# Kernel tuning notes

Hardware: AMD Instinct MI355X
Metric: run time of the kernel (lower is better)

The kernel has to match this reference:

```python
import jax, jax.numpy as jnp
import numpy as np
from jax import lax


def setup_inputs() -> dict:
    key = jax.random.key(0)
    k1, k2 = jax.random.split(key)
    L, B, D = 1024, 16, 1024
    x = jax.random.normal(k1, (L, B, D), dtype=jnp.float32)
    # weight maps n_in -> n_out*k with k=3 (n_in == n_out); small scale for stability
    weight = jax.random.normal(k2, (D, 3 * D), dtype=jnp.float32) * 0.05
    bias = jnp.zeros((2 * D,), dtype=jnp.float32)
    c0 = jnp.zeros((B, D), dtype=jnp.float32)
    return {"x": x, "weight": weight, "bias": bias, "c0": c0}


def reference(x, weight, bias, c0):
    # SRUCell forward, k == 3 (n_in == n_out), unidirectional, tanh activation,
    # no dropout masks (mask_h == NULL -> mask = 1).
    L, B, D = x.shape
    u = (x.reshape(L * B, D) @ weight).reshape(L, B, D, 3)
    b1 = bias[:D]
    b2 = bias[D:]
    u0 = u[..., 0]                                   # [L, B, D]
    g1 = jax.nn.sigmoid(u[..., 1] + b1)              # forget gate
    g2 = jax.nn.sigmoid(u[..., 2] + b2)              # reset/highway gate

    def step(c, inp):
        u0_t, g1_t, g2_t, x_t = inp
        c_new = (c - u0_t) * g1_t + u0_t             # c = c'*g1 + u0*(1-g1)
        h_t = (jnp.tanh(c_new) - x_t) * g2_t + x_t   # h = act(c)*g2 + x*(1-g2)
        return c_new, h_t

    c_last, h = lax.scan(step, c0, (u0, g1, g2, x))
    return h, c_last
```

## Files before the change

### kernel.cpp

```cpp
#include <hip/hip_runtime.h>

#define L_DIM 1024
#define B_DIM 16
#define D_DIM 1024
#define K_DIM 1024
#define N_DIM 3072
#define M_DIM (L_DIM * B_DIM)
#define CHAINS 16384
#define CHUNK 32
#define NCHUNK 32

typedef float f32x4 __attribute__((ext_vector_type(4)));
typedef __bf16 bf16x8 __attribute__((ext_vector_type(8)));
typedef unsigned short u16;
typedef unsigned int u32;

__device__ __forceinline__ u16 f2bf(float f) {
  u32 u = __float_as_uint(f);
  u = u + 0x7FFFu + ((u >> 16) & 1u);
  return (u16)(u >> 16);
}
__device__ __forceinline__ float bf2f(u16 v) {
  return __uint_as_float(((u32)v) << 16);
}
__device__ __forceinline__ float bf2f_lo(u32 v) {
  return __uint_as_float(v << 16);
}
__device__ __forceinline__ float bf2f_hi(u32 v) {
  return __uint_as_float(v & 0xffff0000u);
}
__device__ __forceinline__ float fexp(float v) {
  return __builtin_amdgcn_exp2f(v * 1.4426950408889634f);
}
__device__ __forceinline__ float sigm(float z) {
  return __builtin_amdgcn_rcpf(1.0f + fexp(-z));
}
__device__ __forceinline__ float ftanh(float v) {
  return 1.0f - 2.0f * __builtin_amdgcn_rcpf(1.0f + fexp(2.0f * v));
}

__global__ __launch_bounds__(256) void cvt_x_kernel(const float4* __restrict__ in,
                                                    ushort4* __restrict__ out, int n4) {
  int i = blockIdx.x * 256 + threadIdx.x;
  if (i < n4) {
    float4 v = in[i];
    ushort4 o;
    o.x = f2bf(v.x); o.y = f2bf(v.y); o.z = f2bf(v.z); o.w = f2bf(v.w);
    out[i] = o;
  }
}

__global__ __launch_bounds__(256) void cvt_w_kernel(const float* __restrict__ W,
                                                    u16* __restrict__ Wt) {
  __shared__ float tile[64][65];
  int c0 = blockIdx.x * 64;
  int r0 = blockIdx.y * 64;
  int tx = threadIdx.x & 63;
  int ty = threadIdx.x >> 6;
#pragma unroll
  for (int i = 0; i < 16; ++i) {
    int row = i * 4 + ty;
    tile[row][tx] = W[(size_t)(r0 + row) * N_DIM + c0 + tx];
  }
  __syncthreads();
#pragma unroll
  for (int i = 0; i < 16; ++i) {
    int crow = i * 4 + ty;
    int c = c0 + crow;
    int nprime = (c % 3) * D_DIM + (c / 3);
    Wt[(size_t)nprime * K_DIM + r0 + tx] = f2bf(tile[tx][crow]);
  }
}


#define AS1 __attribute__((address_space(1)))
#define AS3 __attribute__((address_space(3)))
#define STAGE(gp, lp) do { \
  __builtin_amdgcn_global_load_lds((const AS1 void*)(gp), (AS3 void*)(lp), 16, 0, 0); \
  __builtin_amdgcn_global_load_lds((const AS1 void*)((gp) + (size_t)64 * K_DIM), \
                                   (AS3 void*)((lp) + 4096), 16, 0, 0); \
} while (0)

#define QUAD(AI, JB, BF) \
  _Pragma("unroll") \
  for (int i = 0; i < 4; ++i) { \
    _Pragma("unroll") \
    for (int j = 0; j < 2; ++j) { \
      acc[AI + i][JB + j] = __builtin_amdgcn_mfma_f32_16x16x32_bf16(aF[i][0], BF[j][0], acc[AI + i][JB + j], 0, 0, 0); \
      acc[AI + i][JB + j] = __builtin_amdgcn_mfma_f32_16x16x32_bf16(aF[i][1], BF[j][1], acc[AI + i][JB + j], 0, 0, 0); \
    } \
  }

__global__ __launch_bounds__(512, 2) void gemm_kernel(const u16* __restrict__ A,
                                                      const u16* __restrict__ Bt,
                                                      u16* __restrict__ U) {
  __shared__ __align__(16) u16 sm[65536];
  const int tid = threadIdx.x;
  const int wave = tid >> 6;
  const int lane = tid & 63;
  const int wm = wave >> 2;
  const int wn = wave & 3;
  const int quad = lane >> 4;
  const int l16 = lane & 15;

  const int flat = blockIdx.y * 12 + blockIdx.x;
  const int swz = (flat & 7) * 96 + (flat >> 3);
  const int m0 = (swz / 12) * 256;
  const int n0 = (swz % 12) * 256;

  const int rr = tid >> 3;
  const int slot = (tid & 7) ^ (rr & 7);
  const u16* gA = A + (size_t)(m0 + rr) * K_DIM + slot * 8;
  const u16* gB = Bt + (size_t)(n0 + rr) * K_DIM + slot * 8;

  u16* ldsA = sm + wave * 512;
  u16* ldsB = sm + 32768 + wave * 512;

  const int swzu = (l16 & 7) << 3;
  const int c0 = (quad * 8) ^ swzu;
  const int c1 = (32 + quad * 8) ^ swzu;
  const u16* pA = sm + (wm * 128 + l16) * 64;
  const u16* pB = sm + 32768 + (wn * 64 + l16) * 64;

  f32x4 acc[8][4] = {};

  STAGE(gA, ldsA);
  STAGE(gA + (size_t)128 * K_DIM, ldsA + 8192);
  STAGE(gB, ldsB);
  STAGE(gB + (size_t)128 * K_DIM, ldsB + 8192);
  STAGE(gB + 64, ldsB + 16384);
  STAGE(gB + (size_t)128 * K_DIM + 64, ldsB + 16384 + 8192);
  asm volatile("s_waitcnt vmcnt(0)" ::: "memory");
  __builtin_amdgcn_s_barrier();

  for (int u = 0; u < 16; ++u) {
    const int buf = u & 1;
    const int nb = buf ^ 1;
    const u16* pAb = pA + buf * 16384;
    const u16* pBb = pB + buf * 16384;
    bf16x8 aF[4][2], bLo[2][2], bHi[2][2];

#pragma unroll
    for (int i = 0; i < 4; ++i) {
      aF[i][0] = *(const bf16x8*)(pAb + i * 1024 + c0);
      aF[i][1] = *(const bf16x8*)(pAb + i * 1024 + c1);
    }
#pragma unroll
    for (int j = 0; j < 2; ++j) {
      bLo[j][0] = *(const bf16x8*)(pBb + j * 1024 + c0);
      bLo[j][1] = *(const bf16x8*)(pBb + j * 1024 + c1);
    }
    if (u < 15) STAGE(gA + (u + 1) * 64, ldsA + nb * 16384);
    __builtin_amdgcn_s_barrier();
    __builtin_amdgcn_s_setprio(1);
    QUAD(0, 0, bLo)
    __builtin_amdgcn_s_setprio(0);
    __builtin_amdgcn_s_barrier();

#pragma unroll
    for (int j = 0; j < 2; ++j) {
      bHi[j][0] = *(const bf16x8*)(pBb + (2 + j) * 1024 + c0);
      bHi[j][1] = *(const bf16x8*)(pBb + (2 + j) * 1024 + c1);
    }
    if (u < 15) STAGE(gA + (size_t)128 * K_DIM + (u + 1) * 64, ldsA + nb * 16384 + 8192);
    __builtin_amdgcn_s_barrier();
    __builtin_amdgcn_s_setprio(1);
    QUAD(0, 2, bHi)
    __builtin_amdgcn_s_setprio(0);
    __builtin_amdgcn_s_barrier();

#pragma unroll
    for (int i = 0; i < 4; ++i) {
      aF[i][0] = *(const bf16x8*)(pAb + (4 + i) * 1024 + c0);
      aF[i][1] = *(const bf16x8*)(pAb + (4 + i) * 1024 + c1);
    }
    if (u < 14) STAGE(gB + (u + 2) * 64, ldsB + buf * 16384);
    __builtin_amdgcn_s_barrier();
    __builtin_amdgcn_s_setprio(1);
    QUAD(4, 2, bHi)
    __builtin_amdgcn_s_setprio(0);
    __builtin_amdgcn_s_barrier();

    if (u < 14) {
      STAGE(gB + (size_t)128 * K_DIM + (u + 2) * 64, ldsB + buf * 16384 + 8192);
      asm volatile("s_waitcnt vmcnt(4)" ::: "memory");
    } else if (u == 14) {
      asm volatile("s_waitcnt vmcnt(0)" ::: "memory");
    }
    __builtin_amdgcn_s_barrier();
    __builtin_amdgcn_s_setprio(1);
    QUAD(4, 0, bLo)
    __builtin_amdgcn_s_setprio(0);
    __builtin_amdgcn_s_barrier();
  }

#pragma unroll
  for (int i = 0; i < 8; ++i) {
#pragma unroll
    for (int j = 0; j < 4; ++j) {
      const int col = n0 + wn * 64 + j * 16 + l16;
      const int rb = m0 + wm * 128 + i * 16 + quad * 4;
#pragma unroll
      for (int r = 0; r < 4; ++r)
        U[(size_t)(rb + r) * N_DIM + col] = f2bf(acc[i][j][r]);
    }
  }
}


__global__ __launch_bounds__(512) void sru_fused(const u16* __restrict__ U,
                                                 const float* __restrict__ x,
                                                 const float* __restrict__ bias,
                                                 const float* __restrict__ c0,
                                                 float* __restrict__ h,
                                                 float* __restrict__ clast) {
  __shared__ float sA[NCHUNK][32];
  __shared__ float sB[NCHUNK][32];
  __shared__ float sC[NCHUNK][32];

  const int flat = blockIdx.x;
  const int cb = (flat & 7) * 64 + (flat >> 3);
  const int b  = cb >> 5;
  const int d0 = (cb & 31) << 5;
  const int t  = threadIdx.x;
  const int pr = t & 15;
  const int j  = t >> 4;
  const int d2 = d0 + pr * 2;

  const float2 bb1 = *(const float2*)(bias + d2);

  {
    const u16* p = U + (size_t)(j * CHUNK * B_DIM + b) * N_DIM + d2;
    float A0 = 1.0f, A1 = 1.0f, B0 = 0.0f, B1 = 0.0f;
#pragma unroll 4
    for (int s = 0; s < CHUNK; ++s) {
      u32 w0 = *(const u32*)p;
      u32 w1 = *(const u32*)(p + D_DIM);
      float u0a = bf2f_lo(w0), u0b = bf2f_hi(w0);
      float g1a = sigm(bf2f_lo(w1) + bb1.x);
      float g1b = sigm(bf2f_hi(w1) + bb1.y);
      B0 = (B0 - u0a) * g1a + u0a;
      B1 = (B1 - u0b) * g1b + u0b;
      A0 *= g1a;
      A1 *= g1b;
      p += (size_t)B_DIM * N_DIM;
    }
    *(float2*)&sA[j][pr * 2] = make_float2(A0, A1);
    *(float2*)&sB[j][pr * 2] = make_float2(B0, B1);
  }
  __syncthreads();

  if (t < 32) {
    const int chain = cb * 32 + t;
    float c = c0[chain];
#pragma unroll
    for (int jj = 0; jj < NCHUNK; ++jj) {
      sC[jj][t] = c;
      c = sA[jj][t] * c + sB[jj][t];
    }
    clast[chain] = c;
  }
  __syncthreads();

  {
    const float2 bb2 = *(const float2*)(bias + D_DIM + d2);
    float2 c = *(const float2*)&sC[j][pr * 2];
    const size_t m0 = (size_t)(j * CHUNK * B_DIM + b);
    const u16* p = U + m0 * N_DIM + d2;
    const float* xp = x + m0 * D_DIM + d2;
    float* hp = h + m0 * D_DIM + d2;
#pragma unroll 4
    for (int s = 0; s < CHUNK; ++s) {
      u32 w0 = *(const u32*)p;
      u32 w1 = *(const u32*)(p + D_DIM);
      u32 w2 = *(const u32*)(p + 2 * D_DIM);
      float2 xv = *(const float2*)xp;
      float u0a = bf2f_lo(w0), u0b = bf2f_hi(w0);
      float g1a = sigm(bf2f_lo(w1) + bb1.x);
      float g1b = sigm(bf2f_hi(w1) + bb1.y);
      float g2a = sigm(bf2f_lo(w2) + bb2.x);
      float g2b = sigm(bf2f_hi(w2) + bb2.y);
      c.x = (c.x - u0a) * g1a + u0a;
      c.y = (c.y - u0b) * g1b + u0b;
      float2 hv;
      hv.x = (ftanh(c.x) - xv.x) * g2a + xv.x;
      hv.y = (ftanh(c.y) - xv.y) * g2b + xv.y;
      *(float2*)hp = hv;
      p += (size_t)B_DIM * N_DIM;
      xp += B_DIM * D_DIM;
      hp += B_DIM * D_DIM;
    }
  }
}

extern "C" void kernel_launch(void* const* d_in, const int* in_sizes, int n_in,
                              void* d_out, int out_size, void* d_ws, size_t ws_size,
                              hipStream_t stream) {
  const float* x = (const float*)d_in[0];
  const float* W = (const float*)d_in[1];
  const float* bias = (const float*)d_in[2];
  const float* c0 = (const float*)d_in[3];
  float* out = (float*)d_out;

  char* ws = (char*)d_ws;
  u16* xb = (u16*)ws;
  u16* wt = (u16*)(ws + 33554432);
  u16* U = (u16*)(ws + 33554432 + 6291456);

  cvt_x_kernel<<<16384, 256, 0, stream>>>((const float4*)x, (ushort4*)xb, M_DIM * K_DIM / 4);
  cvt_w_kernel<<<dim3(48, 16), 256, 0, stream>>>(W, wt);
  gemm_kernel<<<dim3(N_DIM / 256, M_DIM / 256), 512, 0, stream>>>(xb, wt, U);
  sru_fused<<<512, 512, 0, stream>>>(U, x, bias, c0, out, out + (size_t)M_DIM * D_DIM);
}
```

Baseline: 285.9 us.

## Fuse fp32-to-bf16 conversion of x into GEMM A-tile loading; widen SRU blocks

Removes the separate cvt_x kernel: the GEMM now loads fp32 x directly into registers, packs it to bf16, and writes it into LDS, instead of using the async global_load_lds path on a prebuilt bf16 copy. This saves a 64MB read plus 32MB write round trip and one launch. The cost is that the GEMM reads twice the A bytes per tile and uses register-staged loads with extra VGPRs and waitcnt logic, which could disturb the MFMA pipeline. The SRU scan kernel also moves to 1024-thread blocks covering 64 channels each, with half as many blocks.

```diff
diff --git a/kernel.cpp b/kernel.cpp
--- a/kernel.cpp
+++ b/kernel.cpp
@@ -38,16 +38,13 @@
 __device__ __forceinline__ float ftanh(float v) {
   return 1.0f - 2.0f * __builtin_amdgcn_rcpf(1.0f + fexp(2.0f * v));
 }
-
-__global__ __launch_bounds__(256) void cvt_x_kernel(const float4* __restrict__ in,
-                                                    ushort4* __restrict__ out, int n4) {
-  int i = blockIdx.x * 256 + threadIdx.x;
-  if (i < n4) {
-    float4 v = in[i];
-    ushort4 o;
-    o.x = f2bf(v.x); o.y = f2bf(v.y); o.z = f2bf(v.z); o.w = f2bf(v.w);
-    out[i] = o;
-  }
+__device__ __forceinline__ uint4 pack8(f32x4 a, f32x4 b) {
+  uint4 r;
+  r.x = (u32)f2bf(a[0]) | ((u32)f2bf(a[1]) << 16);
+  r.y = (u32)f2bf(a[2]) | ((u32)f2bf(a[3]) << 16);
+  r.z = (u32)f2bf(b[0]) | ((u32)f2bf(b[1]) << 16);
+  r.w = (u32)f2bf(b[2]) | ((u32)f2bf(b[3]) << 16);
+  return r;
 }
 
 __global__ __launch_bounds__(256) void cvt_w_kernel(const float* __restrict__ W,
@@ -91,7 +88,7 @@
     } \
   }
 
-__global__ __launch_bounds__(512, 2) void gemm_kernel(const u16* __restrict__ A,
+__global__ __launch_bounds__(512, 2) void gemm_kernel(const float* __restrict__ X,
                                                       const u16* __restrict__ Bt,
                                                       u16* __restrict__ U) {
   __shared__ __align__(16) u16 sm[65536];
@@ -110,11 +107,11 @@
 
   const int rr = tid >> 3;
   const int slot = (tid & 7) ^ (rr & 7);
-  const u16* gA = A + (size_t)(m0 + rr) * K_DIM + slot * 8;
+  const float* gA = X + (size_t)(m0 + rr) * K_DIM + slot * 8;
   const u16* gB = Bt + (size_t)(n0 + rr) * K_DIM + slot * 8;
 
-  u16* ldsA = sm + wave * 512;
   u16* ldsB = sm + 32768 + wave * 512;
+  u16* wrA = sm + tid * 8;
 
   const int swzu = (l16 & 7) << 3;
   const int c0 = (quad * 8) ^ swzu;
@@ -124,13 +121,26 @@
 
   f32x4 acc[8][4] = {};
 
-  STAGE(gA, ldsA);
-  STAGE(gA + (size_t)128 * K_DIM, ldsA + 8192);
-  STAGE(gB, ldsB);
-  STAGE(gB + (size_t)128 * K_DIM, ldsB + 8192);
-  STAGE(gB + 64, ldsB + 16384);
-  STAGE(gB + (size_t)128 * K_DIM + 64, ldsB + 16384 + 8192);
-  asm volatile("s_waitcnt vmcnt(0)" ::: "memory");
+  {
+    f32x4 a0 = *(const f32x4*)(gA);
+    f32x4 a1 = *(const f32x4*)(gA + 4);
+    f32x4 a2 = *(const f32x4*)(gA + (size_t)64 * K_DIM);
+    f32x4 a3 = *(const f32x4*)(gA + (size_t)64 * K_DIM + 4);
+    f32x4 a4 = *(const f32x4*)(gA + (size_t)128 * K_DIM);
+    f32x4 a5 = *(const f32x4*)(gA + (size_t)128 * K_DIM + 4);
+    f32x4 a6 = *(const f32x4*)(gA + (size_t)192 * K_DIM);
+    f32x4 a7 = *(const f32x4*)(gA + (size_t)192 * K_DIM + 4);
+    STAGE(gB, ldsB);
+    STAGE(gB + (size_t)128 * K_DIM, ldsB + 8192);
+    STAGE(gB + 64, ldsB + 16384);
+    STAGE(gB + (size_t)128 * K_DIM + 64, ldsB + 16384 + 8192);
+    asm volatile("s_waitcnt vmcnt(8)" ::: "memory");
+    *(uint4*)(wrA)              = pack8(a0, a1);
+    *(uint4*)(wrA + 4096)       = pack8(a2, a3);
+    *(uint4*)(wrA + 8192)       = pack8(a4, a5);
+    *(uint4*)(wrA + 8192 + 4096) = pack8(a6, a7);
+    asm volatile("s_waitcnt vmcnt(4) lgkmcnt(0)" ::: "memory");
+  }
   __builtin_amdgcn_s_barrier();
 
   for (int u = 0; u < 16; ++u) {
@@ -139,6 +149,7 @@
     const u16* pAb = pA + buf * 16384;
     const u16* pBb = pB + buf * 16384;
     bf16x8 aF[4][2], bLo[2][2], bHi[2][2];
+    f32x4 n0a, n0b, n1a, n1b, n2a, n2b, n3a, n3b;
 
 #pragma unroll
     for (int i = 0; i < 4; ++i) {
@@ -150,7 +161,12 @@
       bLo[j][0] = *(const bf16x8*)(pBb + j * 1024 + c0);
       bLo[j][1] = *(const bf16x8*)(pBb + j * 1024 + c1);
     }
-    if (u < 15) STAGE(gA + (u + 1) * 64, ldsA + nb * 16384);
+    if (u < 15) {
+      n0a = *(const f32x4*)(gA + (u + 1) * 64);
+      n0b = *(const f32x4*)(gA + (u + 1) * 64 + 4);
+      n1a = *(const f32x4*)(gA + (size_t)64 * K_DIM + (u + 1) * 64);
+      n1b = *(const f32x4*)(gA + (size_t)64 * K_DIM + (u + 1) * 64 + 4);
+    }
     __builtin_amdgcn_s_barrier();
     __builtin_amdgcn_s_setprio(1);
     QUAD(0, 0, bLo)
@@ -162,7 +178,12 @@
       bHi[j][0] = *(const bf16x8*)(pBb + (2 + j) * 1024 + c0);
       bHi[j][1] = *(const bf16x8*)(pBb + (2 + j) * 1024 + c1);
     }
-    if (u < 15) STAGE(gA + (size_t)128 * K_DIM + (u + 1) * 64, ldsA + nb * 16384 + 8192);
+    if (u < 15) {
+      n2a = *(const f32x4*)(gA + (size_t)128 * K_DIM + (u + 1) * 64);
+      n2b = *(const f32x4*)(gA + (size_t)128 * K_DIM + (u + 1) * 64 + 4);
+      n3a = *(const f32x4*)(gA + (size_t)192 * K_DIM + (u + 1) * 64);
+      n3b = *(const f32x4*)(gA + (size_t)192 * K_DIM + (u + 1) * 64 + 4);
+    }
     __builtin_amdgcn_s_barrier();
     __builtin_amdgcn_s_setprio(1);
     QUAD(0, 2, bHi)
@@ -187,6 +208,14 @@
     } else if (u == 14) {
       asm volatile("s_waitcnt vmcnt(0)" ::: "memory");
     }
+    if (u < 15) {
+      u16* wA = wrA + nb * 16384;
+      *(uint4*)(wA)              = pack8(n0a, n0b);
+      *(uint4*)(wA + 4096)       = pack8(n1a, n1b);
+      *(uint4*)(wA + 8192)       = pack8(n2a, n2b);
+      *(uint4*)(wA + 8192 + 4096) = pack8(n3a, n3b);
+      asm volatile("s_waitcnt lgkmcnt(0)" ::: "memory");
+    }
     __builtin_amdgcn_s_barrier();
     __builtin_amdgcn_s_setprio(1);
     QUAD(4, 0, bLo)
@@ -208,23 +237,23 @@
 }
 
 
-__global__ __launch_bounds__(512) void sru_fused(const u16* __restrict__ U,
-                                                 const float* __restrict__ x,
-                                                 const float* __restrict__ bias,
-                                                 const float* __restrict__ c0,
-                                                 float* __restrict__ h,
-                                                 float* __restrict__ clast) {
-  __shared__ float sA[NCHUNK][32];
-  __shared__ float sB[NCHUNK][32];
-  __shared__ float sC[NCHUNK][32];
+__global__ __launch_bounds__(1024) void sru_fused(const u16* __restrict__ U,
+                                                  const float* __restrict__ x,
+                                                  const float* __restrict__ bias,
+                                                  const float* __restrict__ c0,
+                                                  float* __restrict__ h,
+                                                  float* __restrict__ clast) {
+  __shared__ float sA[NCHUNK][64];
+  __shared__ float sB[NCHUNK][64];
+  __shared__ float sC[NCHUNK][64];
 
   const int flat = blockIdx.x;
-  const int cb = (flat & 7) * 64 + (flat >> 3);
-  const int b  = cb >> 5;
-  const int d0 = (cb & 31) << 5;
+  const int cb = (flat & 7) * 32 + (flat >> 3);
+  const int b  = cb >> 4;
+  const int d0 = (cb & 15) << 6;
   const int t  = threadIdx.x;
-  const int pr = t & 15;
-  const int j  = t >> 4;
+  const int pr = t & 31;
+  const int j  = t >> 5;
   const int d2 = d0 + pr * 2;
 
   const float2 bb1 = *(const float2*)(bias + d2);
@@ -250,8 +279,8 @@
   }
   __syncthreads();
 
-  if (t < 32) {
-    const int chain = cb * 32 + t;
+  if (t < 64) {
+    const int chain = cb * 64 + t;
     float c = c0[chain];
 #pragma unroll
     for (int jj = 0; jj < NCHUNK; ++jj) {
@@ -303,12 +332,10 @@
   float* out = (float*)d_out;
 
   char* ws = (char*)d_ws;
-  u16* xb = (u16*)ws;
-  u16* wt = (u16*)(ws + 33554432);
-  u16* U = (u16*)(ws + 33554432 + 6291456);
-
-  cvt_x_kernel<<<16384, 256, 0, stream>>>((const float4*)x, (ushort4*)xb, M_DIM * K_DIM / 4);
+  u16* wt = (u16*)ws;
+  u16* U = (u16*)(ws + 8388608);
+
   cvt_w_kernel<<<dim3(48, 16), 256, 0, stream>>>(W, wt);
-  gemm_kernel<<<dim3(N_DIM / 256, M_DIM / 256), 512, 0, stream>>>(xb, wt, U);
-  sru_fused<<<512, 512, 0, stream>>>(U, x, bias, c0, out, out + (size_t)M_DIM * D_DIM);
-}
+  gemm_kernel<<<dim3(N_DIM / 256, M_DIM / 256), 512, 0, stream>>>(x, wt, U);
+  sru_fused<<<256, 1024, 0, stream>>>(U, x, bias, c0, out, out + (size_t)M_DIM * D_DIM);
+}
```

Result: slower. 302.0 us (+5.6%).

## Widen SRU scan to four channels per thread with shorter chunks

Applied to the files above, without the earlier changes.

Each thread of the chunked-scan kernel now handles four adjacent channels with 8-byte bf16 and 16-byte fp32 loads instead of two. The time dimension is split into 64 chunks of 16 steps rather than 32 of 32, and blocks grow to 1024 threads covering 64 chains, with half as many blocks launched. This is meant to cut per-thread sequential latency and widen memory transactions. In exchange the serial cross-chunk combine gets twice as long, and the larger blocks mean fewer blocks in flight.

```diff
diff --git a/kernel.cpp b/kernel.cpp
--- a/kernel.cpp
+++ b/kernel.cpp
@@ -7,8 +7,8 @@
 #define N_DIM 3072
 #define M_DIM (L_DIM * B_DIM)
 #define CHAINS 16384
-#define CHUNK 32
-#define NCHUNK 32
+#define CHUNK 16
+#define NCHUNK 64
 
 typedef float f32x4 __attribute__((ext_vector_type(4)));
 typedef __bf16 bf16x8 __attribute__((ext_vector_type(8)));
@@ -208,50 +208,54 @@
 }
 
 
-__global__ __launch_bounds__(512) void sru_fused(const u16* __restrict__ U,
-                                                 const float* __restrict__ x,
-                                                 const float* __restrict__ bias,
-                                                 const float* __restrict__ c0,
-                                                 float* __restrict__ h,
-                                                 float* __restrict__ clast) {
-  __shared__ float sA[NCHUNK][32];
-  __shared__ float sB[NCHUNK][32];
-  __shared__ float sC[NCHUNK][32];
+__global__ __launch_bounds__(1024) void sru_fused(const u16* __restrict__ U,
+                                                  const float* __restrict__ x,
+                                                  const float* __restrict__ bias,
+                                                  const float* __restrict__ c0,
+                                                  float* __restrict__ h,
+                                                  float* __restrict__ clast) {
+  __shared__ float sA[NCHUNK][64];
+  __shared__ float sB[NCHUNK][64];
+  __shared__ float sC[NCHUNK][64];
 
   const int flat = blockIdx.x;
-  const int cb = (flat & 7) * 64 + (flat >> 3);
-  const int b  = cb >> 5;
-  const int d0 = (cb & 31) << 5;
+  const int cb = (flat & 7) * 32 + (flat >> 3);
+  const int b  = cb >> 4;
+  const int d0 = (cb & 15) << 6;
   const int t  = threadIdx.x;
-  const int pr = t & 15;
+  const int q  = t & 15;
   const int j  = t >> 4;
-  const int d2 = d0 + pr * 2;
-
-  const float2 bb1 = *(const float2*)(bias + d2);
+  const int d4 = d0 + q * 4;
+
+  const float4 bb1 = *(const float4*)(bias + d4);
 
   {
-    const u16* p = U + (size_t)(j * CHUNK * B_DIM + b) * N_DIM + d2;
-    float A0 = 1.0f, A1 = 1.0f, B0 = 0.0f, B1 = 0.0f;
+    const u16* p = U + (size_t)(j * CHUNK * B_DIM + b) * N_DIM + d4;
+    float A0 = 1.0f, A1 = 1.0f, A2 = 1.0f, A3 = 1.0f;
+    float B0 = 0.0f, B1 = 0.0f, B2 = 0.0f, B3 = 0.0f;
 #pragma unroll 4
     for (int s = 0; s < CHUNK; ++s) {
-      u32 w0 = *(const u32*)p;
-      u32 w1 = *(const u32*)(p + D_DIM);
-      float u0a = bf2f_lo(w0), u0b = bf2f_hi(w0);
-      float g1a = sigm(bf2f_lo(w1) + bb1.x);
-      float g1b = sigm(bf2f_hi(w1) + bb1.y);
-      B0 = (B0 - u0a) * g1a + u0a;
-      B1 = (B1 - u0b) * g1b + u0b;
-      A0 *= g1a;
-      A1 *= g1b;
+      uint2 w0 = *(const uint2*)p;
+      uint2 w1 = *(const uint2*)(p + D_DIM);
+      float u00 = bf2f_lo(w0.x), u01 = bf2f_hi(w0.x);
+      float u02 = bf2f_lo(w0.y), u03 = bf2f_hi(w0.y);
+      float g10 = sigm(bf2f_lo(w1.x) + bb1.x);
+      float g11 = sigm(bf2f_hi(w1.x) + bb1.y);
+      float g12 = sigm(bf2f_lo(w1.y) + bb1.z);
+      float g13 = sigm(bf2f_hi(w1.y) + bb1.w);
+      B0 = (B0 - u00) * g10 + u00;  A0 *= g10;
+      B1 = (B1 - u01) * g11 + u01;  A1 *= g11;
+      B2 = (B2 - u02) * g12 + u02;  A2 *= g12;
+      B3 = (B3 - u03) * g13 + u03;  A3 *= g13;
       p += (size_t)B_DIM * N_DIM;
     }
-    *(float2*)&sA[j][pr * 2] = make_float2(A0, A1);
-    *(float2*)&sB[j][pr * 2] = make_float2(B0, B1);
+    *(float4*)&sA[j][q * 4] = make_float4(A0, A1, A2, A3);
+    *(float4*)&sB[j][q * 4] = make_float4(B0, B1, B2, B3);
   }
   __syncthreads();
 
-  if (t < 32) {
-    const int chain = cb * 32 + t;
+  if (t < 64) {
+    const int chain = cb * 64 + t;
     float c = c0[chain];
 #pragma unroll
     for (int jj = 0; jj < NCHUNK; ++jj) {
@@ -263,29 +267,38 @@
   __syncthreads();
 
   {
-    const float2 bb2 = *(const float2*)(bias + D_DIM + d2);
-    float2 c = *(const float2*)&sC[j][pr * 2];
+    const float4 bb2 = *(const float4*)(bias + D_DIM + d4);
+    float4 c = *(const float4*)&sC[j][q * 4];
     const size_t m0 = (size_t)(j * CHUNK * B_DIM + b);
-    const u16* p = U + m0 * N_DIM + d2;
-    const float* xp = x + m0 * D_DIM + d2;
-    float* hp = h + m0 * D_DIM + d2;
+    const u16* p = U + m0 * N_DIM + d4;
+    const float* xp = x + m0 * D_DIM + d4;
+    float* hp = h + m0 * D_DIM + d4;
 #pragma unroll 4
     for (int s = 0; s < CHUNK; ++s) {
-      u32 w0 = *(const u32*)p;
-      u32 w1 = *(const u32*)(p + D_DIM);
-      u32 w2 = *(const u32*)(p + 2 * D_DIM);
-      float2 xv = *(const float2*)xp;
-      float u0a = bf2f_lo(w0), u0b = bf2f_hi(w0);
-      float g1a = sigm(bf2f_lo(w1) + bb1.x);
-      float g1b = sigm(bf2f_hi(w1) + bb1.y);
-      float g2a = sigm(bf2f_lo(w2) + bb2.x);
-      float g2b = sigm(bf2f_hi(w2) + bb2.y);
-      c.x = (c.x - u0a) * g1a + u0a;
-      c.y = (c.y - u0b) * g1b + u0b;
-      float2 hv;
-      hv.x = (ftanh(c.x) - xv.x) * g2a + xv.x;
-      hv.y = (ftanh(c.y) - xv.y) * g2b + xv.y;
-      *(float2*)hp = hv;
+      uint2 w0 = *(const uint2*)p;
+      uint2 w1 = *(const uint2*)(p + D_DIM);
+      uint2 w2 = *(const uint2*)(p + 2 * D_DIM);
+      float4 xv = *(const float4*)xp;
+      float u00 = bf2f_lo(w0.x), u01 = bf2f_hi(w0.x);
+      float u02 = bf2f_lo(w0.y), u03 = bf2f_hi(w0.y);
+      float g10 = sigm(bf2f_lo(w1.x) + bb1.x);
+      float g11 = sigm(bf2f_hi(w1.x) + bb1.y);
+      float g12 = sigm(bf2f_lo(w1.y) + bb1.z);
+      float g13 = sigm(bf2f_hi(w1.y) + bb1.w);
+      float g20 = sigm(bf2f_lo(w2.x) + bb2.x);
+      float g21 = sigm(bf2f_hi(w2.x) + bb2.y);
+      float g22 = sigm(bf2f_lo(w2.y) + bb2.z);
+      float g23 = sigm(bf2f_hi(w2.y) + bb2.w);
+      c.x = (c.x - u00) * g10 + u00;
+      c.y = (c.y - u01) * g11 + u01;
+      c.z = (c.z - u02) * g12 + u02;
+      c.w = (c.w - u03) * g13 + u03;
+      float4 hv;
+      hv.x = (ftanh(c.x) - xv.x) * g20 + xv.x;
+      hv.y = (ftanh(c.y) - xv.y) * g21 + xv.y;
+      hv.z = (ftanh(c.z) - xv.z) * g22 + xv.z;
+      hv.w = (ftanh(c.w) - xv.w) * g23 + xv.w;
+      *(float4*)hp = hv;
       p += (size_t)B_DIM * N_DIM;
       xp += B_DIM * D_DIM;
       hp += B_DIM * D_DIM;
@@ -310,5 +323,5 @@
   cvt_x_kernel<<<16384, 256, 0, stream>>>((const float4*)x, (ushort4*)xb, M_DIM * K_DIM / 4);
   cvt_w_kernel<<<dim3(48, 16), 256, 0, stream>>>(W, wt);
   gemm_kernel<<<dim3(N_DIM / 256, M_DIM / 256), 512, 0, stream>>>(xb, wt, U);
-  sru_fused<<<512, 512, 0, stream>>>(U, x, bias, c0, out, out + (size_t)M_DIM * D_DIM);
-}
+  sru_fused<<<256, 1024, 0, stream>>>(U, x, bias, c0, out, out + (size_t)M_DIM * D_DIM);
+}
```

Result: faster. 270.9 us (-5.2%).
